# Performance work log

Measured on AMD Instinct MI355X. Metric: run time of the kernel, lower is better.

Reference implementation:

```python
import jax, jax.numpy as jnp
import numpy as np
from jax import lax

B, C, H, W = 8, 128, 128, 128
HEADS = 16
HEAD_C = C // HEADS  # 8
SLOPE = 0.2
EPS = 1e-12


def _conv(x, w, b, padding, groups=1):
    # x: [B,C,H,W], w: [O,I/groups,kh,kw]
    y = lax.conv_general_dilated(
        x, w, window_strides=(1, 1), padding=padding,
        dimension_numbers=("NCHW", "OIHW", "NCHW"),
        feature_group_count=groups)
    return y + b[None, :, None, None]


def _conv_block(x, conv1_w, conv1_b, conv2_w, conv2_b, dw_w, dw_b, sc_w, sc_b):
    h = _conv(x, conv1_w, conv1_b, ((1, 1), (1, 1)))            # 3x3, zero pad
    h = jnp.where(h >= 0, h, SLOPE * h)                          # LeakyReLU
    h = _conv(h, conv2_w, conv2_b, ((0, 0), (0, 0)))             # 1x1
    hp = jnp.pad(h, ((0, 0), (0, 0), (1, 1), (1, 1)), mode="reflect")
    h = _conv(hp, dw_w, dw_b, ((0, 0), (0, 0)), groups=C)        # depthwise 3x3, reflect pad
    h = jnp.where(h >= 0, h, SLOPE * h)
    sc = _conv(x, sc_w, sc_b, ((0, 0), (0, 0)))                  # 1x1 shortcut
    return h + sc


def setup_inputs() -> dict:
    key = jax.random.key(0)
    ks = jax.random.split(key, 10)
    s = 0.05
    return {
        "x1": jax.random.normal(ks[0], (B, C, H, W), jnp.float32),
        "x2": jax.random.normal(ks[1], (B, C, H, W), jnp.float32),
        "temperature": jnp.ones((HEADS, 1, 1), jnp.float32),
        "conv1_w": jax.random.normal(ks[2], (C, C, 3, 3), jnp.float32) * s,
        "conv1_b": jnp.zeros((C,), jnp.float32),
        "conv2_w": jax.random.normal(ks[3], (C, C, 1, 1), jnp.float32) * s,
        "conv2_b": jnp.zeros((C,), jnp.float32),
        "dw_w": jax.random.normal(ks[4], (C, 1, 3, 3), jnp.float32) * s,
        "dw_b": jnp.zeros((C,), jnp.float32),
        "sc_w": jax.random.normal(ks[5], (C, C, 1, 1), jnp.float32) * s,
        "sc_b": jnp.zeros((C,), jnp.float32),
    }


def reference(x1, x2, temperature, conv1_w, conv1_b, conv2_w, conv2_b,
              dw_w, dw_b, sc_w, sc_b):
    b, c, h, w = x2.shape
    # b (head c) h w -> b head c (h w)
    qk = x1.reshape(b, HEADS, HEAD_C, h * w)
    v = x2.reshape(b, HEADS, HEAD_C, h * w)
    # L2-normalize over spatial dim (F.normalize, eps=1e-12)
    norm = jnp.sqrt(jnp.sum(qk * qk, axis=-1, keepdims=True))
    qn = qk / jnp.maximum(norm, EPS)
    # channel attention: [b, head, c, c]
    attn = jnp.einsum("bhcn,bhdn->bhcd", qn, qn) * temperature
    attn = jax.nn.softmax(attn, axis=-1)
    out = jnp.einsum("bhcd,bhdn->bhcn", attn, v)
    out = out.reshape(b, c, h, w)
    out = _conv_block(out, conv1_w, conv1_b, conv2_w, conv2_b,
                      dw_w, dw_b, sc_w, sc_b)
    return out + x1
```

## Files before the change

kernel.cpp:

```cpp
#include <hip/hip_runtime.h>
#include <hip/hip_bf16.h>

typedef __attribute__((ext_vector_type(8))) short short8;
typedef __attribute__((ext_vector_type(4))) float f32x4;

#define NB 8
#define NC 128
#define NHW 128
#define NSP (NHW*NHW)
#define SLOPE 0.2f
#define EPSN 1e-12f
#define PADW 130

static __device__ __forceinline__ unsigned short f2bf(float f) {
    __hip_bfloat16 h = __float2bfloat16(f);
    return *reinterpret_cast<unsigned short*>(&h);
}
static __device__ __forceinline__ float bf2f(__hip_bfloat16 h) {
    return __bfloat162float(h);
}

__global__ void prep_wb1(const float* __restrict__ w, __hip_bfloat16* __restrict__ wb) {
    int idx = blockIdx.x * 256 + threadIdx.x;
    if (idx >= 128 * 128 * 9) return;
    int kw = idx % 3; int t = idx / 3;
    int kh = t % 3;   t /= 3;
    int i  = t % 128; int o = t / 128;
    int tap = kh * 3 + kw;
    int half = i >> 6, icc = (i >> 5) & 1, lk = (i >> 3) & 3, j = i & 7;
    int wn = o >> 6, c = (o >> 4) & 3, l15 = o & 15;
    int lane = lk * 16 + l15;
    size_t chunk = (size_t)tap * 32 + half * 16 + wn * 8 + icc * 4 + c;
    wb[chunk * 512 + lane * 8 + j] = __float2bfloat16(w[idx]);
}

__global__ void prep_w1x1(const float* __restrict__ w, __hip_bfloat16* __restrict__ wb) {
    int idx = blockIdx.x * 256 + threadIdx.x;
    if (idx >= 128 * 128) return;
    int i = idx & 127, o = idx >> 7;
    int kk = i >> 5, lk = (i >> 3) & 3, j = i & 7;
    int wn = o >> 6, c = (o >> 4) & 3, l15 = o & 15;
    int lane = lk * 16 + l15;
    size_t chunk = ((size_t)(wn * 4 + kk) * 4 + c);
    wb[chunk * 512 + lane * 8 + j] = __float2bfloat16(w[idx]);
}

__global__ void pad_zero(__hip_bfloat16* __restrict__ yt2) {
    int t = blockIdx.x * 256 + threadIdx.x;
    if (t >= 8 * 516) return;
    int b = t / 516, s = t % 516;
    int row, col;
    if (s < 130)      { row = 0;           col = s; }
    else if (s < 260) { row = 129;         col = s - 130; }
    else if (s < 388) { row = s - 260 + 1; col = 0; }
    else              { row = s - 388 + 1; col = 129; }
    uint4* dst = reinterpret_cast<uint4*>(yt2 + ((size_t)(b * PADW + row) * PADW + col) * 128);
    uint4 z = make_uint4(0u, 0u, 0u, 0u);
#pragma unroll
    for (int i = 0; i < 16; ++i) dst[i] = z;
}

__global__ __launch_bounds__(256) void gram_part(const float* __restrict__ x1,
                                                 float* __restrict__ Gp) {
    int bh = blockIdx.x & 127;
    int q  = blockIdx.x >> 7;
    const float* base = x1 + (size_t)bh * 8 * NSP + q * 4096;
    float acc[8][8];
#pragma unroll
    for (int c = 0; c < 8; c++)
#pragma unroll
        for (int d = 0; d < 8; d++) acc[c][d] = 0.f;

    for (int n = threadIdx.x; n < 4096; n += 256) {
        float v[8];
#pragma unroll
        for (int c = 0; c < 8; c++) v[c] = base[c * NSP + n];
#pragma unroll
        for (int c = 0; c < 8; c++)
#pragma unroll
            for (int d = 0; d < 8; d++)
                acc[c][d] = fmaf(v[c], v[d], acc[c][d]);
    }
#pragma unroll
    for (int c = 0; c < 8; c++)
#pragma unroll
        for (int d = 0; d < 8; d++)
            for (int off = 32; off > 0; off >>= 1)
                acc[c][d] += __shfl_down(acc[c][d], off);

    __shared__ float red[4][64];
    int wv = threadIdx.x >> 6;
    if ((threadIdx.x & 63) == 0) {
#pragma unroll
        for (int c = 0; c < 8; c++)
#pragma unroll
            for (int d = 0; d < 8; d++) red[wv][c * 8 + d] = acc[c][d];
    }
    __syncthreads();
    if (threadIdx.x < 64)
        Gp[(size_t)(q * 128 + bh) * 64 + threadIdx.x] =
            red[0][threadIdx.x] + red[1][threadIdx.x] + red[2][threadIdx.x] + red[3][threadIdx.x];
}

__global__ void gram_reduce(const float* __restrict__ Gp, float* __restrict__ G) {
    int bh = blockIdx.x;
    int t = threadIdx.x;
    float s = 0.f;
#pragma unroll
    for (int q = 0; q < 4; q++) s += Gp[(size_t)(q * 128 + bh) * 64 + t];
    G[bh * 64 + t] = s;
}

__global__ void softmax_kernel(const float* __restrict__ G, const float* __restrict__ temp,
                               float* __restrict__ attn) {
    int bh = blockIdx.x; int h = bh & 15;
    int t = threadIdx.x;
    int c = t >> 3, d = t & 7;
    const float* g = G + bh * 64;
    float nc = fmaxf(sqrtf(g[c * 8 + c]), EPSN);
    float nd = fmaxf(sqrtf(g[d * 8 + d]), EPSN);
    float a = g[t] / (nc * nd) * temp[h];
    float m = a;
#pragma unroll
    for (int off = 4; off > 0; off >>= 1) m = fmaxf(m, __shfl_xor(m, off));
    float e = __expf(a - m);
    float s = e;
#pragma unroll
    for (int off = 4; off > 0; off >>= 1) s += __shfl_xor(s, off);
    attn[bh * 64 + t] = e / s;
}

__global__ __launch_bounds__(256) void av_v3(const float* __restrict__ x2,
                                             const float* __restrict__ attn,
                                             __hip_bfloat16* __restrict__ yt2) {
    int b  = blockIdx.x >> 8;
    int p0 = (blockIdx.x & 255) << 6;
    __shared__ float vt[128][65];
    __shared__ float at[16][65];
    for (int idx = threadIdx.x; idx < 1024; idx += 256)
        at[idx >> 6][idx & 63] = attn[(size_t)b * 1024 + idx];
    for (int idx = threadIdx.x; idx < 8192; idx += 256) {
        int row = idx >> 6, col = idx & 63;
        vt[row][col] = x2[(size_t)(b * 128 + row) * NSP + p0 + col];
    }
    __syncthreads();
    for (int idx = threadIdx.x; idx < 1024; idx += 256) {
        int cq = idx & 15;
        int p  = idx >> 4;
        float vv[8];
#pragma unroll
        for (int d = 0; d < 8; d++) vv[d] = vt[cq * 8 + d][p];
        unsigned int pk[4];
#pragma unroll
        for (int c = 0; c < 8; c += 2) {
            float s0 = 0.f, s1 = 0.f;
#pragma unroll
            for (int d = 0; d < 8; d++) {
                s0 = fmaf(at[cq][c * 8 + d], vv[d], s0);
                s1 = fmaf(at[cq][(c + 1) * 8 + d], vv[d], s1);
            }
            pk[c >> 1] = (unsigned int)f2bf(s0) | ((unsigned int)f2bf(s1) << 16);
        }
        uint4 st; st.x = pk[0]; st.y = pk[1]; st.z = pk[2]; st.w = pk[3];
        int n = p0 + p;
        int hh = n >> 7, wc = n & 127;
        *reinterpret_cast<uint4*>(
            yt2 + ((size_t)(b * PADW + hh + 1) * PADW + wc + 1) * 128 + cq * 8) = st;
    }
}

#define BPTR(s) (wf1 + ((size_t)(((((s) % 18) >> 1) * 32) + ((s) / 18) * 16 + wn * 8 + ((s) & 1) * 4)) * 64 + lane)

__global__ __launch_bounds__(256, 4) void fused_conv(const __hip_bfloat16* __restrict__ yt2,
                                                     const __hip_bfloat16* __restrict__ wb1,
                                                     const __hip_bfloat16* __restrict__ wb2,
                                                     const __hip_bfloat16* __restrict__ wbsc,
                                                     const float* __restrict__ b1,
                                                     const float* __restrict__ b2,
                                                     const float* __restrict__ bsc,
                                                     const float* __restrict__ x1,
                                                     __hip_bfloat16* __restrict__ h2,
                                                     float* __restrict__ out) {
    __shared__ uint4 smem[1584];
    char* smem_raw = (char*)smem;
    int bid = blockIdx.x;
    int swz = (bid & 7) * 256 + (bid >> 3);
    int b = swz >> 8;
    int rh = swz & 255;
    int h = rh >> 1;
    int p0 = (rh & 1) * 64;
    int tid = threadIdx.x;
    int lane = tid & 63;
    int wid = tid >> 6;
    int wm = wid >> 1, wn = wid & 1;
    int l15 = lane & 15;
    int lk = lane >> 4;

    const short8* wf1  = reinterpret_cast<const short8*>(wb1);
    const short8* wf2  = reinterpret_cast<const short8*>(wb2);
    const short8* wfsc = reinterpret_cast<const short8*>(wbsc);

    f32x4 acc[2][4];
#pragma unroll
    for (int a = 0; a < 2; a++)
#pragma unroll
        for (int c = 0; c < 4; c++) acc[a][c] = (f32x4){0.f, 0.f, 0.f, 0.f};

    const short8* wpi = BPTR(0);
    short8 bA0 = wpi[0], bA1 = wpi[64], bA2 = wpi[128], bA3 = wpi[192];
    wpi = BPTR(1);
    short8 bB0 = wpi[0], bB1 = wpi[64], bB2 = wpi[128], bB3 = wpi[192];

#pragma unroll
    for (int half = 0; half < 2; ++half) {
        __syncthreads();
        for (int idx = tid; idx < 1584; idx += 256) {
            int g = idx & 7;
            int colr = idx >> 3;
            int col = colr % 66;
            int r = colr / 66;
            uint4 v = *reinterpret_cast<const uint4*>(
                yt2 + ((size_t)(b * PADW + h + r) * PADW + (p0 + col)) * 128 + half * 64 + g * 8);
            smem[(r * 66 + col) * 8 + (g ^ (col & 7))] = v;
        }
        __syncthreads();

#pragma unroll
        for (int gp = 0; gp < 9; ++gp) {
            const int kh = gp / 3, kw = gp - kh * 3;
            {
                const int s = half * 18 + gp * 2;
                short8 n0, n1, n2, n3;
                const bool more = (s + 2 < 36);
                if (more) {
                    const short8* w2 = BPTR(s + 2);
                    n0 = w2[0]; n1 = w2[64]; n2 = w2[128]; n3 = w2[192];
                }
                short8 afr[2];
#pragma unroll
                for (int a = 0; a < 2; ++a) {
                    int col = (wm * 2 + a) * 16 + l15 + kw;
                    int g = lk;
                    afr[a] = *reinterpret_cast<const short8*>(
                        &smem[(kh * 66 + col) * 8 + (g ^ (col & 7))]);
                }
                __builtin_amdgcn_s_setprio(1);
#pragma unroll
                for (int a = 0; a < 2; ++a) {
                    acc[a][0] = __builtin_amdgcn_mfma_f32_16x16x32_bf16(afr[a], bA0, acc[a][0], 0, 0, 0);
                    acc[a][1] = __builtin_amdgcn_mfma_f32_16x16x32_bf16(afr[a], bA1, acc[a][1], 0, 0, 0);
                    acc[a][2] = __builtin_amdgcn_mfma_f32_16x16x32_bf16(afr[a], bA2, acc[a][2], 0, 0, 0);
                    acc[a][3] = __builtin_amdgcn_mfma_f32_16x16x32_bf16(afr[a], bA3, acc[a][3], 0, 0, 0);
                }
                __builtin_amdgcn_s_setprio(0);
                if (more) { bA0 = n0; bA1 = n1; bA2 = n2; bA3 = n3; }
            }
            {
                const int s = half * 18 + gp * 2 + 1;
                short8 n0, n1, n2, n3;
                const bool more = (s + 2 < 36);
                if (more) {
                    const short8* w2 = BPTR(s + 2);
                    n0 = w2[0]; n1 = w2[64]; n2 = w2[128]; n3 = w2[192];
                }
                short8 afr[2];
#pragma unroll
                for (int a = 0; a < 2; ++a) {
                    int col = (wm * 2 + a) * 16 + l15 + kw;
                    int g = 4 + lk;
                    afr[a] = *reinterpret_cast<const short8*>(
                        &smem[(kh * 66 + col) * 8 + (g ^ (col & 7))]);
                }
                __builtin_amdgcn_s_setprio(1);
#pragma unroll
                for (int a = 0; a < 2; ++a) {
                    acc[a][0] = __builtin_amdgcn_mfma_f32_16x16x32_bf16(afr[a], bB0, acc[a][0], 0, 0, 0);
                    acc[a][1] = __builtin_amdgcn_mfma_f32_16x16x32_bf16(afr[a], bB1, acc[a][1], 0, 0, 0);
                    acc[a][2] = __builtin_amdgcn_mfma_f32_16x16x32_bf16(afr[a], bB2, acc[a][2], 0, 0, 0);
                    acc[a][3] = __builtin_amdgcn_mfma_f32_16x16x32_bf16(afr[a], bB3, acc[a][3], 0, 0, 0);
                }
                __builtin_amdgcn_s_setprio(0);
                if (more) { bB0 = n0; bB1 = n1; bB2 = n2; bB3 = n3; }
            }
        }
    }

    __syncthreads();
#pragma unroll
    for (int c = 0; c < 4; ++c) {
        int o = wn * 64 + c * 16 + l15;
        float bv = b1[o];
        int go = o >> 3, ob = (o & 7) << 1;
#pragma unroll
        for (int a = 0; a < 2; ++a) {
            int pb = (wm * 2 + a) * 16 + lk * 4;
#pragma unroll
            for (int j = 0; j < 4; ++j) {
                int p = pb + j;
                float v = acc[a][c][j] + bv;
                v = v >= 0.f ? v : SLOPE * v;
                *reinterpret_cast<__hip_bfloat16*>(
                    smem_raw + p * 256 + (((go ^ (p & 15)) << 4) | ob)) = __float2bfloat16(v);
            }
        }
    }
    __syncthreads();

#pragma unroll
    for (int a = 0; a < 2; a++)
#pragma unroll
        for (int c = 0; c < 4; c++) acc[a][c] = (f32x4){0.f, 0.f, 0.f, 0.f};
#pragma unroll
    for (int kk = 0; kk < 4; ++kk) {
        short8 bfr[4];
#pragma unroll
        for (int c = 0; c < 4; ++c)
            bfr[c] = wf2[((size_t)(wn * 4 + kk) * 4 + c) * 64 + lane];
        short8 afr[2];
        int g = kk * 4 + lk;
#pragma unroll
        for (int a = 0; a < 2; ++a) {
            int p = (wm * 2 + a) * 16 + l15;
            afr[a] = *reinterpret_cast<const short8*>(smem_raw + p * 256 + ((g ^ (p & 15)) << 4));
        }
        __builtin_amdgcn_s_setprio(1);
#pragma unroll
        for (int a = 0; a < 2; ++a)
#pragma unroll
            for (int c = 0; c < 4; ++c)
                acc[a][c] = __builtin_amdgcn_mfma_f32_16x16x32_bf16(afr[a], bfr[c], acc[a][c], 0, 0, 0);
        __builtin_amdgcn_s_setprio(0);
    }
#pragma unroll
    for (int c = 0; c < 4; ++c) {
        int o = wn * 64 + c * 16 + l15;
        float bv = b2[o];
        size_t obase = ((size_t)(b * 128 + o) * 128 + h) * 128 + p0;
#pragma unroll
        for (int a = 0; a < 2; ++a) {
            int w0 = (wm * 2 + a) * 16 + lk * 4;
            uint2 st;
            st.x = (unsigned int)f2bf(acc[a][c][0] + bv) | ((unsigned int)f2bf(acc[a][c][1] + bv) << 16);
            st.y = (unsigned int)f2bf(acc[a][c][2] + bv) | ((unsigned int)f2bf(acc[a][c][3] + bv) << 16);
            *reinterpret_cast<uint2*>(h2 + obase + w0) = st;
        }
    }

    __syncthreads();
    for (int idx = tid; idx < 1024; idx += 256) {
        int p = idx >> 4, g = idx & 15;
        uint4 v = *reinterpret_cast<const uint4*>(
            yt2 + ((size_t)(b * PADW + h + 1) * PADW + (p0 + 1 + p)) * 128 + g * 8);
        *reinterpret_cast<uint4*>(smem_raw + p * 256 + ((g ^ (p & 15)) << 4)) = v;
    }
    __syncthreads();

#pragma unroll
    for (int a = 0; a < 2; a++)
#pragma unroll
        for (int c = 0; c < 4; c++) acc[a][c] = (f32x4){0.f, 0.f, 0.f, 0.f};
#pragma unroll
    for (int kk = 0; kk < 4; ++kk) {
        short8 bfr[4];
#pragma unroll
        for (int c = 0; c < 4; ++c)
            bfr[c] = wfsc[((size_t)(wn * 4 + kk) * 4 + c) * 64 + lane];
        short8 afr[2];
        int g = kk * 4 + lk;
#pragma unroll
        for (int a = 0; a < 2; ++a) {
            int p = (wm * 2 + a) * 16 + l15;
            afr[a] = *reinterpret_cast<const short8*>(smem_raw + p * 256 + ((g ^ (p & 15)) << 4));
        }
        __builtin_amdgcn_s_setprio(1);
#pragma unroll
        for (int a = 0; a < 2; ++a)
#pragma unroll
            for (int c = 0; c < 4; ++c)
                acc[a][c] = __builtin_amdgcn_mfma_f32_16x16x32_bf16(afr[a], bfr[c], acc[a][c], 0, 0, 0);
        __builtin_amdgcn_s_setprio(0);
    }
#pragma unroll
    for (int c = 0; c < 4; ++c) {
        int o = wn * 64 + c * 16 + l15;
        float bv = bsc[o];
        size_t obase = ((size_t)(b * 128 + o) * 128 + h) * 128 + p0;
#pragma unroll
        for (int a = 0; a < 2; ++a) {
            int w0 = (wm * 2 + a) * 16 + lk * 4;
            float4 xv = *reinterpret_cast<const float4*>(x1 + obase + w0);
            float4 st;
            st.x = acc[a][c][0] + bv + xv.x;
            st.y = acc[a][c][1] + bv + xv.y;
            st.z = acc[a][c][2] + bv + xv.z;
            st.w = acc[a][c][3] + bv + xv.w;
            *reinterpret_cast<float4*>(out + obase + w0) = st;
        }
    }
}

__global__ __launch_bounds__(256) void dw_v2(const __hip_bfloat16* __restrict__ h2,
                                             const float* __restrict__ dww,
                                             const float* __restrict__ dwb,
                                             float* __restrict__ out) {
    int bid = blockIdx.x;
    int swz = (bid & 7) * 1024 + (bid >> 3);
    size_t tidx = (size_t)swz * 256 + threadIdx.x;
    int w0 = (int)((tidx & 15) << 3);
    int hh = (int)((tidx >> 4) & 127);
    int bc = (int)(tidx >> 11);
    int c  = bc & 127;
    const __hip_bfloat16* src = h2 + ((size_t)bc << 14);
    float wg[9];
#pragma unroll
    for (int k = 0; k < 9; ++k) wg[k] = dww[c * 9 + k];
    float bv = dwb[c];
    float a8[8];
#pragma unroll
    for (int j = 0; j < 8; ++j) a8[j] = bv;
#pragma unroll
    for (int kh = 0; kh < 3; ++kh) {
        int ih = hh + kh - 1;
        ih = ih < 0 ? 1 : (ih > 127 ? 126 : ih);
        const __hip_bfloat16* row = src + ih * 128;
        short8 mid = *reinterpret_cast<const short8*>(row + w0);
        float v[10];
        v[0] = bf2f(row[w0 == 0 ? 1 : w0 - 1]);
#pragma unroll
        for (int j = 0; j < 8; ++j)
            v[j + 1] = __uint_as_float((unsigned int)(unsigned short)mid[j] << 16);
        v[9] = bf2f(row[w0 == 120 ? 126 : w0 + 8]);
#pragma unroll
        for (int kw = 0; kw < 3; ++kw)
#pragma unroll
            for (int j = 0; j < 8; ++j)
                a8[j] = fmaf(v[j + kw], wg[kh * 3 + kw], a8[j]);
    }
    size_t ob = ((size_t)bc << 14) + hh * 128 + w0;
    float4 o0 = *reinterpret_cast<const float4*>(out + ob);
    float4 o1 = *reinterpret_cast<const float4*>(out + ob + 4);
#pragma unroll
    for (int j = 0; j < 8; ++j) a8[j] = a8[j] >= 0.f ? a8[j] : SLOPE * a8[j];
    o0.x += a8[0]; o0.y += a8[1]; o0.z += a8[2]; o0.w += a8[3];
    o1.x += a8[4]; o1.y += a8[5]; o1.z += a8[6]; o1.w += a8[7];
    *reinterpret_cast<float4*>(out + ob) = o0;
    *reinterpret_cast<float4*>(out + ob + 4) = o1;
}

extern "C" void kernel_launch(void* const* d_in, const int* in_sizes, int n_in,
                              void* d_out, int out_size, void* d_ws, size_t ws_size,
                              hipStream_t stream) {
    const float* x1   = (const float*)d_in[0];
    const float* x2   = (const float*)d_in[1];
    const float* temp = (const float*)d_in[2];
    const float* c1w  = (const float*)d_in[3];
    const float* c1b  = (const float*)d_in[4];
    const float* c2w  = (const float*)d_in[5];
    const float* c2b  = (const float*)d_in[6];
    const float* dww  = (const float*)d_in[7];
    const float* dwb  = (const float*)d_in[8];
    const float* scw  = (const float*)d_in[9];
    const float* scb  = (const float*)d_in[10];
    float* out = (float*)d_out;
    char* ws = (char*)d_ws;

    float*          G    = (float*)(ws);
    float*          attn = (float*)(ws + (32 << 10));
    float*          Gp   = (float*)(ws + (64 << 10));
    __hip_bfloat16* wb1  = (__hip_bfloat16*)(ws + (192 << 10));
    __hip_bfloat16* wb2  = (__hip_bfloat16*)(ws + (480 << 10));
    __hip_bfloat16* wbsc = (__hip_bfloat16*)(ws + (512 << 10));
    __hip_bfloat16* yt2  = (__hip_bfloat16*)(ws + ((size_t)1 << 20));
    __hip_bfloat16* h2b  = (__hip_bfloat16*)(ws + ((size_t)36 << 20));

    prep_wb1<<<576, 256, 0, stream>>>(c1w, wb1);
    prep_w1x1<<<64, 256, 0, stream>>>(c2w, wb2);
    prep_w1x1<<<64, 256, 0, stream>>>(scw, wbsc);
    pad_zero<<<17, 256, 0, stream>>>(yt2);

    gram_part<<<512, 256, 0, stream>>>(x1, Gp);
    gram_reduce<<<128, 64, 0, stream>>>(Gp, G);
    softmax_kernel<<<128, 64, 0, stream>>>(G, temp, attn);
    av_v3<<<2048, 256, 0, stream>>>(x2, attn, yt2);

    fused_conv<<<2048, 256, 0, stream>>>(yt2, wb1, wb2, wbsc, c1b, c2b, scb, x1, h2b, out);
    dw_v2<<<8192, 256, 0, stream>>>(h2b, dww, dwb, out);
}
```

Baseline: 167.7 us.

## Merge prep kernels, fold gram reduce into softmax, stage shortcut as bf16

Combines the three weight-prep kernels and the pad-zero kernel into one launch, and folds the Gram partial reduction into the softmax kernel to cut launch count. The shortcut conv output is now written as bf16 to a scratch buffer instead of fp32 into out. The residual add with x1 moves into the depthwise kernel, so out is written once rather than written and then read-modify-written. This trades fp32 shortcut precision for lower memory traffic.

After: 162.6 us. -3.0%, faster.

```diff
diff --git a/kernel.cpp b/kernel.cpp
--- a/kernel.cpp
+++ b/kernel.cpp
@@ -20,44 +20,45 @@
     return __bfloat162float(h);
 }
 
-__global__ void prep_wb1(const float* __restrict__ w, __hip_bfloat16* __restrict__ wb) {
+__global__ void prep_all(const float* __restrict__ c1w, const float* __restrict__ c2w,
+                         const float* __restrict__ scw,
+                         __hip_bfloat16* __restrict__ wb1, __hip_bfloat16* __restrict__ wb2,
+                         __hip_bfloat16* __restrict__ wbsc, __hip_bfloat16* __restrict__ yt2) {
     int idx = blockIdx.x * 256 + threadIdx.x;
-    if (idx >= 128 * 128 * 9) return;
-    int kw = idx % 3; int t = idx / 3;
-    int kh = t % 3;   t /= 3;
-    int i  = t % 128; int o = t / 128;
-    int tap = kh * 3 + kw;
-    int half = i >> 6, icc = (i >> 5) & 1, lk = (i >> 3) & 3, j = i & 7;
-    int wn = o >> 6, c = (o >> 4) & 3, l15 = o & 15;
-    int lane = lk * 16 + l15;
-    size_t chunk = (size_t)tap * 32 + half * 16 + wn * 8 + icc * 4 + c;
-    wb[chunk * 512 + lane * 8 + j] = __float2bfloat16(w[idx]);
-}
-
-__global__ void prep_w1x1(const float* __restrict__ w, __hip_bfloat16* __restrict__ wb) {
-    int idx = blockIdx.x * 256 + threadIdx.x;
-    if (idx >= 128 * 128) return;
-    int i = idx & 127, o = idx >> 7;
-    int kk = i >> 5, lk = (i >> 3) & 3, j = i & 7;
-    int wn = o >> 6, c = (o >> 4) & 3, l15 = o & 15;
-    int lane = lk * 16 + l15;
-    size_t chunk = ((size_t)(wn * 4 + kk) * 4 + c);
-    wb[chunk * 512 + lane * 8 + j] = __float2bfloat16(w[idx]);
-}
-
-__global__ void pad_zero(__hip_bfloat16* __restrict__ yt2) {
-    int t = blockIdx.x * 256 + threadIdx.x;
-    if (t >= 8 * 516) return;
-    int b = t / 516, s = t % 516;
-    int row, col;
-    if (s < 130)      { row = 0;           col = s; }
-    else if (s < 260) { row = 129;         col = s - 130; }
-    else if (s < 388) { row = s - 260 + 1; col = 0; }
-    else              { row = s - 388 + 1; col = 129; }
-    uint4* dst = reinterpret_cast<uint4*>(yt2 + ((size_t)(b * PADW + row) * PADW + col) * 128);
-    uint4 z = make_uint4(0u, 0u, 0u, 0u);
-#pragma unroll
-    for (int i = 0; i < 16; ++i) dst[i] = z;
+    if (idx < 147456) {
+        int kw = idx % 3; int t = idx / 3;
+        int kh = t % 3;   t /= 3;
+        int i  = t % 128; int o = t / 128;
+        int tap = kh * 3 + kw;
+        int half = i >> 6, icc = (i >> 5) & 1, lk = (i >> 3) & 3, j = i & 7;
+        int wn = o >> 6, c = (o >> 4) & 3, l15 = o & 15;
+        int lane = lk * 16 + l15;
+        size_t chunk = (size_t)tap * 32 + half * 16 + wn * 8 + icc * 4 + c;
+        wb1[chunk * 512 + lane * 8 + j] = __float2bfloat16(c1w[idx]);
+    } else if (idx < 180224) {
+        int i2 = idx - 147456;
+        const float* src = (i2 < 16384) ? c2w : scw;
+        __hip_bfloat16* dst = (i2 < 16384) ? wb2 : wbsc;
+        int e = i2 & 16383;
+        int i = e & 127, o = e >> 7;
+        int kk = i >> 5, lk = (i >> 3) & 3, j = i & 7;
+        int wn = o >> 6, c = (o >> 4) & 3, l15 = o & 15;
+        int lane = lk * 16 + l15;
+        size_t chunk = ((size_t)(wn * 4 + kk) * 4 + c);
+        dst[chunk * 512 + lane * 8 + j] = __float2bfloat16(src[e]);
+    } else if (idx < 184352) {
+        int t = idx - 180224;
+        int b = t / 516, s = t % 516;
+        int row, col;
+        if (s < 130)      { row = 0;           col = s; }
+        else if (s < 260) { row = 129;         col = s - 130; }
+        else if (s < 388) { row = s - 260 + 1; col = 0; }
+        else              { row = s - 388 + 1; col = 129; }
+        uint4* dst = reinterpret_cast<uint4*>(yt2 + ((size_t)(b * PADW + row) * PADW + col) * 128);
+        uint4 z = make_uint4(0u, 0u, 0u, 0u);
+#pragma unroll
+        for (int i = 0; i < 16; ++i) dst[i] = z;
+    }
 }
 
 __global__ __launch_bounds__(256) void gram_part(const float* __restrict__ x1,
@@ -102,24 +103,20 @@
             red[0][threadIdx.x] + red[1][threadIdx.x] + red[2][threadIdx.x] + red[3][threadIdx.x];
 }
 
-__global__ void gram_reduce(const float* __restrict__ Gp, float* __restrict__ G) {
-    int bh = blockIdx.x;
+__global__ void softmax_kernel(const float* __restrict__ Gp, const float* __restrict__ temp,
+                               float* __restrict__ attn) {
+    int bh = blockIdx.x; int hd = bh & 15;
     int t = threadIdx.x;
-    float s = 0.f;
-#pragma unroll
-    for (int q = 0; q < 4; q++) s += Gp[(size_t)(q * 128 + bh) * 64 + t];
-    G[bh * 64 + t] = s;
-}
-
-__global__ void softmax_kernel(const float* __restrict__ G, const float* __restrict__ temp,
-                               float* __restrict__ attn) {
-    int bh = blockIdx.x; int h = bh & 15;
-    int t = threadIdx.x;
+    float g = 0.f;
+#pragma unroll
+    for (int q = 0; q < 4; q++) g += Gp[(size_t)(q * 128 + bh) * 64 + t];
+    __shared__ float gs[64];
+    gs[t] = g;
+    __syncthreads();
     int c = t >> 3, d = t & 7;
-    const float* g = G + bh * 64;
-    float nc = fmaxf(sqrtf(g[c * 8 + c]), EPSN);
-    float nd = fmaxf(sqrtf(g[d * 8 + d]), EPSN);
-    float a = g[t] / (nc * nd) * temp[h];
+    float nc = fmaxf(sqrtf(gs[c * 8 + c]), EPSN);
+    float nd = fmaxf(sqrtf(gs[d * 8 + d]), EPSN);
+    float a = g / (nc * nd) * temp[hd];
     float m = a;
 #pragma unroll
     for (int off = 4; off > 0; off >>= 1) m = fmaxf(m, __shfl_xor(m, off));
@@ -178,9 +175,8 @@
                                                      const float* __restrict__ b1,
                                                      const float* __restrict__ b2,
                                                      const float* __restrict__ bsc,
-                                                     const float* __restrict__ x1,
                                                      __hip_bfloat16* __restrict__ h2,
-                                                     float* __restrict__ out) {
+                                                     __hip_bfloat16* __restrict__ scp) {
     __shared__ uint4 smem[1584];
     char* smem_raw = (char*)smem;
     int bid = blockIdx.x;
@@ -388,18 +384,17 @@
 #pragma unroll
         for (int a = 0; a < 2; ++a) {
             int w0 = (wm * 2 + a) * 16 + lk * 4;
-            float4 xv = *reinterpret_cast<const float4*>(x1 + obase + w0);
-            float4 st;
-            st.x = acc[a][c][0] + bv + xv.x;
-            st.y = acc[a][c][1] + bv + xv.y;
-            st.z = acc[a][c][2] + bv + xv.z;
-            st.w = acc[a][c][3] + bv + xv.w;
-            *reinterpret_cast<float4*>(out + obase + w0) = st;
-        }
-    }
-}
-
-__global__ __launch_bounds__(256) void dw_v2(const __hip_bfloat16* __restrict__ h2,
+            uint2 st;
+            st.x = (unsigned int)f2bf(acc[a][c][0] + bv) | ((unsigned int)f2bf(acc[a][c][1] + bv) << 16);
+            st.y = (unsigned int)f2bf(acc[a][c][2] + bv) | ((unsigned int)f2bf(acc[a][c][3] + bv) << 16);
+            *reinterpret_cast<uint2*>(scp + obase + w0) = st;
+        }
+    }
+}
+
+__global__ __launch_bounds__(256) void dw_v3(const __hip_bfloat16* __restrict__ h2,
+                                             const __hip_bfloat16* __restrict__ scp,
+                                             const float* __restrict__ x1,
                                              const float* __restrict__ dww,
                                              const float* __restrict__ dwb,
                                              float* __restrict__ out) {
@@ -437,12 +432,20 @@
                 a8[j] = fmaf(v[j + kw], wg[kh * 3 + kw], a8[j]);
     }
     size_t ob = ((size_t)bc << 14) + hh * 128 + w0;
-    float4 o0 = *reinterpret_cast<const float4*>(out + ob);
-    float4 o1 = *reinterpret_cast<const float4*>(out + ob + 4);
+    short8 sv = *reinterpret_cast<const short8*>(scp + ob);
+    float4 xa = *reinterpret_cast<const float4*>(x1 + ob);
+    float4 xb = *reinterpret_cast<const float4*>(x1 + ob + 4);
 #pragma unroll
     for (int j = 0; j < 8; ++j) a8[j] = a8[j] >= 0.f ? a8[j] : SLOPE * a8[j];
-    o0.x += a8[0]; o0.y += a8[1]; o0.z += a8[2]; o0.w += a8[3];
-    o1.x += a8[4]; o1.y += a8[5]; o1.z += a8[6]; o1.w += a8[7];
+    float4 o0, o1;
+    o0.x = xa.x + __uint_as_float((unsigned int)(unsigned short)sv[0] << 16) + a8[0];
+    o0.y = xa.y + __uint_as_float((unsigned int)(unsigned short)sv[1] << 16) + a8[1];
+    o0.z = xa.z + __uint_as_float((unsigned int)(unsigned short)sv[2] << 16) + a8[2];
+    o0.w = xa.w + __uint_as_float((unsigned int)(unsigned short)sv[3] << 16) + a8[3];
+    o1.x = xb.x + __uint_as_float((unsigned int)(unsigned short)sv[4] << 16) + a8[4];
+    o1.y = xb.y + __uint_as_float((unsigned int)(unsigned short)sv[5] << 16) + a8[5];
+    o1.z = xb.z + __uint_as_float((unsigned int)(unsigned short)sv[6] << 16) + a8[6];
+    o1.w = xb.w + __uint_as_float((unsigned int)(unsigned short)sv[7] << 16) + a8[7];
     *reinterpret_cast<float4*>(out + ob) = o0;
     *reinterpret_cast<float4*>(out + ob + 4) = o1;
 }
@@ -464,7 +467,6 @@
     float* out = (float*)d_out;
     char* ws = (char*)d_ws;
 
-    float*          G    = (float*)(ws);
     float*          attn = (float*)(ws + (32 << 10));
     float*          Gp   = (float*)(ws + (64 << 10));
     __hip_bfloat16* wb1  = (__hip_bfloat16*)(ws + (192 << 10));
@@ -472,17 +474,14 @@
     __hip_bfloat16* wbsc = (__hip_bfloat16*)(ws + (512 << 10));
     __hip_bfloat16* yt2  = (__hip_bfloat16*)(ws + ((size_t)1 << 20));
     __hip_bfloat16* h2b  = (__hip_bfloat16*)(ws + ((size_t)36 << 20));
-
-    prep_wb1<<<576, 256, 0, stream>>>(c1w, wb1);
-    prep_w1x1<<<64, 256, 0, stream>>>(c2w, wb2);
-    prep_w1x1<<<64, 256, 0, stream>>>(scw, wbsc);
-    pad_zero<<<17, 256, 0, stream>>>(yt2);
+    __hip_bfloat16* scp  = (__hip_bfloat16*)(ws + ((size_t)68 << 20));
+
+    prep_all<<<721, 256, 0, stream>>>(c1w, c2w, scw, wb1, wb2, wbsc, yt2);
 
     gram_part<<<512, 256, 0, stream>>>(x1, Gp);
-    gram_reduce<<<128, 64, 0, stream>>>(Gp, G);
-    softmax_kernel<<<128, 64, 0, stream>>>(G, temp, attn);
+    softmax_kernel<<<128, 64, 0, stream>>>(Gp, temp, attn);
     av_v3<<<2048, 256, 0, stream>>>(x2, attn, yt2);
 
-    fused_conv<<<2048, 256, 0, stream>>>(yt2, wb1, wb2, wbsc, c1b, c2b, scb, x1, h2b, out);
-    dw_v2<<<8192, 256, 0, stream>>>(h2b, dww, dwb, out);
-}
+    fused_conv<<<2048, 256, 0, stream>>>(yt2, wb1, wb2, wbsc, c1b, c2b, scb, h2b, scp);
+    dw_v3<<<8192, 256, 0, stream>>>(h2b, scp, x1, dww, dwb, out);
+}
```
